# Kernel tuning notes

Measured on AMD Instinct MI355X. Metric: run time of the kernel, lower is better.

Reference implementation:

```python
import jax, jax.numpy as jnp
import numpy as np
import math

B, S, E = 16, 600, 300   # batch, seq_len, enc_len
H, NC = 512, 2           # hidden, classes
D = S * E                # archi[0] = 180000


def setup_inputs() -> dict:
    key = jax.random.key(0)
    ks = jax.random.split(key, 7)
    x = jax.random.normal(ks[0], (B, S, E), dtype=jnp.float32)
    y = jax.random.randint(ks[1], (B,), 0, NC)
    # neurons initialized to zeros (init_neurons)
    n0 = jnp.zeros((B, S, E), jnp.float32)
    n1 = jnp.zeros((B, H), jnp.float32)
    n2 = jnp.zeros((B, NC), jnp.float32)
    # Linear weights (torch layout: [out, in]), Kaiming-uniform-like scale 1/sqrt(fan_in)
    W0 = jax.random.uniform(ks[2], (E, E), jnp.float32, -1.0, 1.0) / math.sqrt(E)
    W1 = jax.random.uniform(ks[3], (H, D), jnp.float32, -1.0, 1.0) / math.sqrt(D)
    b1 = jax.random.uniform(ks[4], (H,), jnp.float32, -1.0, 1.0) / math.sqrt(D)
    W2 = jax.random.uniform(ks[5], (NC, H), jnp.float32, -1.0, 1.0) / math.sqrt(H)
    b2 = jax.random.uniform(ks[6], (NC,), jnp.float32, -1.0, 1.0) / math.sqrt(H)
    return dict(x=x, y=y, n0=n0, n1=n1, n2=n2, W0=W0, W1=W1, b1=b1, W2=W2, b2=b2, T=3)


def reference(x, y, n0, n1, n2, W0, W1, b1, W2, b2, T):
    # EqProp free-phase relaxation (beta = 0.0, forward default).
    # Analytic dPhi/dneurons replaces torch.autograd.grad:
    scale = 1.0 / math.sqrt(E)
    Wx = jnp.einsum('bse,fe->bsf', x, W0)  # synapses[0](x), constant across steps
    for _ in range(T):
        g0 = Wx + (n1 @ W1).reshape(B, S, E)              # dPhi/dn0
        g1 = n0.reshape(B, D) @ W1.T + b1 + n2 @ W2       # dPhi/dn1
        g2 = n1 @ W2.T + b2                               # dPhi/dn2 (beta=0)
        # hand-coded attention update for neuron 0: Q=g0, K=V=x
        attn = jax.nn.softmax(scale * jnp.einsum('bse,bte->bst', g0, x), axis=-1)
        n0 = jnp.einsum('bst,bte->bse', attn, x)
        n1 = jnp.tanh(g1)
        n2 = jnp.tanh(g2)
    return n0, n1, n2
```

## Files before the change

kernel.cpp:

```cpp
#include <hip/hip_runtime.h>
#include <math.h>

#define DD 180000L
#define HH 512
#define BB 16
#define SS 600
#define EE 300
#define SP 608
#define EP 320

typedef unsigned short u16;
typedef __attribute__((ext_vector_type(8))) __bf16 bf16x8;
typedef __attribute__((ext_vector_type(4))) float f32x4;

__device__ __forceinline__ u16 f2bf(float f) {
  union { float f; unsigned int u; } x; x.f = f;
  unsigned int r = (x.u + 0x7FFFu + ((x.u >> 16) & 1u)) >> 16;
  return (u16)r;
}

__global__ __launch_bounds__(256) void k_conv_x(const float* __restrict__ x,
                                                u16* __restrict__ xb, u16* __restrict__ xt) {
  __shared__ u16 tl[32][33];
  int b = blockIdx.z;
  int tt = blockIdx.x * 32, ee = blockIdx.y * 32;
  int lx = threadIdx.x & 31, ly = threadIdx.x >> 5;
#pragma unroll
  for (int i = 0; i < 4; ++i) {
    int t = tt + ly + i * 8, e = ee + lx;
    float v = (t < SS && e < EE) ? x[((long)b * SS + t) * EE + e] : 0.f;
    u16 h = f2bf(v);
    xb[((long)b * SP + t) * EP + e] = h;
    tl[ly + i * 8][lx] = h;
  }
  __syncthreads();
#pragma unroll
  for (int i = 0; i < 4; ++i) {
    int e = ee + ly + i * 8, t = tt + lx;
    xt[((long)b * EP + e) * SP + t] = tl[lx][ly + i * 8];
  }
}

__global__ __launch_bounds__(256) void k_conv_w0(const float* __restrict__ W0, u16* __restrict__ w0b) {
  int idx = blockIdx.x * 256 + threadIdx.x;
  int f = idx / EP, e = idx % EP;
  float v = (f < EE && e < EE) ? W0[f * EE + e] : 0.f;
  w0b[idx] = f2bf(v);
}

__global__ __launch_bounds__(256) void k_gemm_nt(
    const u16* __restrict__ A, int lda, long sA, int Arows,
    const u16* __restrict__ B, int ldb, long sB, int Brows,
    float* __restrict__ C, int ldc, long sC, int Mv, int Nv, int K,
    u16* __restrict__ Cb, int ldcb, long sCb) {
  int bz = blockIdx.z;
  int m0 = blockIdx.x * 64, n0 = blockIdx.y * 64;
  int lane = threadIdx.x & 63, wv = threadIdx.x >> 6;
  int wm = m0 + (wv >> 1) * 32, wn = n0 + (wv & 1) * 32;
  int q = lane >> 4, ln = lane & 15;
  const u16* Ab = A + (long)bz * sA;
  const u16* Bb = B + (long)bz * sB;
  long arow0 = (long)min(wm + ln, Arows - 1) * lda;
  long arow1 = (long)min(wm + 16 + ln, Arows - 1) * lda;
  long brow0 = (long)min(wn + ln, Brows - 1) * ldb;
  long brow1 = (long)min(wn + 16 + ln, Brows - 1) * ldb;
  f32x4 acc00 = {0.f,0.f,0.f,0.f}, acc01 = acc00, acc10 = acc00, acc11 = acc00;
  int ksteps = (K + 31) >> 5;
  for (int kk = 0; kk < ksteps; ++kk) {
    int k0 = kk * 32 + q * 8;
    bf16x8 a0 = *(const bf16x8*)(Ab + arow0 + k0);
    bf16x8 a1 = *(const bf16x8*)(Ab + arow1 + k0);
    bf16x8 b0 = *(const bf16x8*)(Bb + brow0 + k0);
    bf16x8 bv1 = *(const bf16x8*)(Bb + brow1 + k0);
    acc00 = __builtin_amdgcn_mfma_f32_16x16x32_bf16(a0, b0,  acc00, 0, 0, 0);
    acc01 = __builtin_amdgcn_mfma_f32_16x16x32_bf16(a0, bv1, acc01, 0, 0, 0);
    acc10 = __builtin_amdgcn_mfma_f32_16x16x32_bf16(a1, b0,  acc10, 0, 0, 0);
    acc11 = __builtin_amdgcn_mfma_f32_16x16x32_bf16(a1, bv1, acc11, 0, 0, 0);
  }
  float* Cp = C + (long)bz * sC;
  u16* Cbp = Cb ? (Cb + (long)bz * sCb) : (u16*)0;
#pragma unroll
  for (int sm = 0; sm < 2; ++sm) {
#pragma unroll
    for (int sn = 0; sn < 2; ++sn) {
      f32x4 acc = (sm == 0) ? ((sn == 0) ? acc00 : acc01) : ((sn == 0) ? acc10 : acc11);
#pragma unroll
      for (int r = 0; r < 4; ++r) {
        int m = wm + sm * 16 + q * 4 + r;
        int n = wn + sn * 16 + ln;
        if (m < Mv) {
          float v = acc[r];
          if (n < Nv) Cp[(long)m * ldc + n] = v;
          if (Cbp && n < ldcb) Cbp[(long)m * ldcb + n] = f2bf(n < Nv ? v : 0.f);
        }
      }
    }
  }
}

#define BN 256
#define BK 64
#define NCH 704

__global__ __launch_bounds__(256) void k_fused_w1(
    const float* __restrict__ W1, const float* __restrict__ n1f,
    const float* __restrict__ n0f, const float* __restrict__ Wx,
    u16* __restrict__ g0b, float* __restrict__ part) {
  __shared__ u16 wt[BK][BN + 8];
  __shared__ u16 n1s[BB][HH + 8];
  __shared__ u16 n0s[BB][BN + 8];
  int tid = threadIdx.x;
  long d0 = (long)blockIdx.x * BN;
#pragma unroll
  for (int i = 0; i < 8; ++i) {
    int f = i * 256 + tid;
    int b = f >> 7, c = (f & 127) * 4;
    float4 v = *(const float4*)(n1f + b * HH + c);
    n1s[b][c] = f2bf(v.x); n1s[b][c + 1] = f2bf(v.y);
    n1s[b][c + 2] = f2bf(v.z); n1s[b][c + 3] = f2bf(v.w);
  }
#pragma unroll
  for (int i = 0; i < 4; ++i) {
    int f = i * 256 + tid;
    int b = f >> 6, c = (f & 63) * 4;
    long d = d0 + c;
    float4 v = {0.f,0.f,0.f,0.f};
    if (d < DD) v = *(const float4*)(n0f + (long)b * DD + d);
    n0s[b][c] = f2bf(v.x); n0s[b][c + 1] = f2bf(v.y);
    n0s[b][c + 2] = f2bf(v.z); n0s[b][c + 3] = f2bf(v.w);
  }
  int lane = tid & 63, wv = tid >> 6, q = lane >> 4, ln = lane & 15;
  f32x4 acc0[4] = {{0.f,0.f,0.f,0.f},{0.f,0.f,0.f,0.f},{0.f,0.f,0.f,0.f},{0.f,0.f,0.f,0.f}};

  float4 pre[16];
#pragma unroll
  for (int i = 0; i < 16; ++i) {
    int f = i * 256 + tid;
    int r = f >> 6, c = (f & 63) * 4;
    long d = d0 + c;
    float4 v = {0.f,0.f,0.f,0.f};
    if (d < DD) v = *(const float4*)(W1 + (long)r * DD + d);
    pre[i] = v;
  }
  for (int s = 0; s < 8; ++s) {
    int h0 = s * BK;
    __syncthreads();
#pragma unroll
    for (int i = 0; i < 16; ++i) {
      int f = i * 256 + tid;
      int r = f >> 6, c = (f & 63) * 4;
      wt[r][c] = f2bf(pre[i].x); wt[r][c + 1] = f2bf(pre[i].y);
      wt[r][c + 2] = f2bf(pre[i].z); wt[r][c + 3] = f2bf(pre[i].w);
    }
    if (s < 7) {
#pragma unroll
      for (int i = 0; i < 16; ++i) {
        int f = i * 256 + tid;
        int r = f >> 6, c = (f & 63) * 4;
        long d = d0 + c;
        float4 v = {0.f,0.f,0.f,0.f};
        if (d < DD) v = *(const float4*)(W1 + (long)(h0 + BK + r) * DD + d);
        pre[i] = v;
      }
    }
    __syncthreads();
#pragma unroll
    for (int kst = 0; kst < 2; ++kst) {
      bf16x8 af = *(const bf16x8*)(&n1s[ln][h0 + kst * 32 + q * 8]);
#pragma unroll
      for (int nt = 0; nt < 4; ++nt) {
        int dc = wv * 64 + nt * 16 + ln;
        bf16x8 bv;
#pragma unroll
        for (int j = 0; j < 8; ++j) bv[j] = *(const __bf16*)(&wt[kst * 32 + q * 8 + j][dc]);
        acc0[nt] = __builtin_amdgcn_mfma_f32_16x16x32_bf16(af, bv, acc0[nt], 0, 0, 0);
      }
    }
    f32x4 acc1 = {0.f,0.f,0.f,0.f};
#pragma unroll
    for (int kst = 0; kst < 8; ++kst) {
      bf16x8 af = *(const bf16x8*)(&n0s[ln][kst * 32 + q * 8]);
      bf16x8 bv = *(const bf16x8*)(&wt[wv * 16 + ln][kst * 32 + q * 8]);
      acc1 = __builtin_amdgcn_mfma_f32_16x16x32_bf16(af, bv, acc1, 0, 0, 0);
    }
    long pb = (long)blockIdx.x * 8192;
#pragma unroll
    for (int r = 0; r < 4; ++r) {
      int b = q * 4 + r, h = h0 + wv * 16 + ln;
      part[pb + b * HH + h] = acc1[r];
    }
  }
#pragma unroll
  for (int nt = 0; nt < 4; ++nt) {
#pragma unroll
    for (int r = 0; r < 4; ++r) {
      int b = q * 4 + r;
      long d = d0 + wv * 64 + nt * 16 + ln;
      if (d < DD) {
        float val = Wx[(long)b * DD + d] + acc0[nt][r];
        int sI = (int)(d / EE), e = (int)(d % EE);
        g0b[((long)b * SS + sI) * EP + e] = f2bf(val);
      }
    }
  }
}

__global__ __launch_bounds__(256) void k_flash(const u16* __restrict__ g0b,
                                               const u16* __restrict__ xb,
                                               const u16* __restrict__ xt,
                                               float* __restrict__ out_n0, float scale) {
  __shared__ u16 Qs[16][328];
  __shared__ float Ss[16][609];
  __shared__ u16 Ps[16][616];
  int qt = blockIdx.x, b = blockIdx.y;
  int tid = threadIdx.x, lane = tid & 63, wv = tid >> 6, q = lane >> 4, ln = lane & 15;

#pragma unroll
  for (int i = 0; i < 3; ++i) {
    int c = tid + i * 256;
    if (c < 640) {
      int row = c / 40, cg = (c % 40) * 8;
      int qrow = min(qt * 16 + row, SS - 1);
      bf16x8 v = *(const bf16x8*)(g0b + ((long)b * SS + qrow) * EP + cg);
#pragma unroll
      for (int j = 0; j < 8; ++j) if (cg + j >= EE) v[j] = (__bf16)0.f;
      *(bf16x8*)&Qs[row][cg] = v;
    }
  }
  __syncthreads();

  f32x4 sacc[10];
#pragma unroll
  for (int i = 0; i < 10; ++i) sacc[i] = (f32x4){0.f,0.f,0.f,0.f};
  for (int k = 0; k < 10; ++k) {
    bf16x8 af = *(const bf16x8*)&Qs[ln][k * 32 + q * 8];
#pragma unroll
    for (int nt = 0; nt < 10; ++nt) {
      int tile = nt * 4 + wv;
      if (tile < 38) {
        bf16x8 bv = *(const bf16x8*)(xb + ((long)b * SP + tile * 16 + ln) * EP + k * 32 + q * 8);
        sacc[nt] = __builtin_amdgcn_mfma_f32_16x16x32_bf16(af, bv, sacc[nt], 0, 0, 0);
      }
    }
  }
#pragma unroll
  for (int nt = 0; nt < 10; ++nt) {
    int tile = nt * 4 + wv;
    if (tile < 38) {
#pragma unroll
      for (int r = 0; r < 4; ++r)
        Ss[q * 4 + r][tile * 16 + ln] = sacc[nt][r] * scale;
    }
  }
  __syncthreads();

#pragma unroll
  for (int r = 0; r < 4; ++r) {
    int row = wv * 4 + r;
    float v[10], mx = -1e30f;
#pragma unroll
    for (int i = 0; i < 10; ++i) {
      int c = lane + i * 64;
      v[i] = (c < SS) ? Ss[row][c] : -1e30f;
      mx = fmaxf(mx, v[i]);
    }
#pragma unroll
    for (int off = 1; off < 64; off <<= 1) mx = fmaxf(mx, __shfl_xor(mx, off));
    float sum = 0.f;
#pragma unroll
    for (int i = 0; i < 10; ++i) {
      int c = lane + i * 64;
      v[i] = (c < SS) ? __expf(v[i] - mx) : 0.f;
      sum += v[i];
    }
#pragma unroll
    for (int off = 1; off < 64; off <<= 1) sum += __shfl_xor(sum, off);
    float inv = 1.f / sum;
#pragma unroll
    for (int i = 0; i < 10; ++i) {
      int c = lane + i * 64;
      if (c < SP) Ps[row][c] = f2bf(v[i] * inv);
    }
  }
  __syncthreads();

  f32x4 oacc[5];
#pragma unroll
  for (int j = 0; j < 5; ++j) oacc[j] = (f32x4){0.f,0.f,0.f,0.f};
  for (int k = 0; k < 19; ++k) {
    bf16x8 af = *(const bf16x8*)&Ps[ln][k * 32 + q * 8];
#pragma unroll
    for (int j = 0; j < 5; ++j) {
      int e = (j * 4 + wv) * 16 + ln;
      bf16x8 bv = *(const bf16x8*)(xt + ((long)b * EP + e) * SP + k * 32 + q * 8);
      oacc[j] = __builtin_amdgcn_mfma_f32_16x16x32_bf16(af, bv, oacc[j], 0, 0, 0);
    }
  }
#pragma unroll
  for (int j = 0; j < 5; ++j) {
    int e = (j * 4 + wv) * 16 + ln;
    if (e < EE) {
#pragma unroll
      for (int r = 0; r < 4; ++r) {
        int qrow = qt * 16 + q * 4 + r;
        if (qrow < SS) out_n0[((long)b * SS + qrow) * EE + e] = oacc[j][r];
      }
    }
  }
}

__global__ __launch_bounds__(256) void k_init(const float* __restrict__ b1, const float* __restrict__ b2,
                                              float* __restrict__ n1, float* __restrict__ n2) {
  int idx = blockIdx.x * 256 + threadIdx.x;
  n1[idx] = tanhf(b1[idx & 511]);
  if (idx < 32) n2[idx] = tanhf(b2[idx & 1]);
}

__global__ __launch_bounds__(64) void k_g2(const float* __restrict__ n1old, const float* __restrict__ W2,
                                           const float* __restrict__ b2, float* __restrict__ n2out) {
  int b = blockIdx.x >> 1, c = blockIdx.x & 1, lane = threadIdx.x;
  float s = 0.f;
#pragma unroll
  for (int i = 0; i < 8; ++i) { int h = lane + i * 64; s += n1old[b * HH + h] * W2[c * HH + h]; }
  for (int off = 32; off; off >>= 1) s += __shfl_down(s, off);
  if (lane == 0) n2out[b * 2 + c] = tanhf(s + b2[c]);
}

__global__ __launch_bounds__(256) void k_reduce1(const float* __restrict__ part, float* __restrict__ part2) {
  int idx = blockIdx.x * 256 + threadIdx.x;
  int sl = blockIdx.y;
  float s = 0.f;
  int c0 = sl * 88;
#pragma unroll 4
  for (int c = 0; c < 88; ++c) s += part[(long)(c0 + c) * 8192 + idx];
  part2[(long)sl * 8192 + idx] = s;
}

__global__ __launch_bounds__(256) void k_reduce2(const float* __restrict__ part2, const float* __restrict__ b1,
                                                 const float* __restrict__ W2, const float* __restrict__ n2old,
                                                 float* __restrict__ n1out) {
  int idx = blockIdx.x * 256 + threadIdx.x;
  int b = idx >> 9, h = idx & 511;
  float s = b1[h] + n2old[b * 2] * W2[h] + n2old[b * 2 + 1] * W2[HH + h];
#pragma unroll
  for (int sl = 0; sl < 8; ++sl) s += part2[(long)sl * 8192 + idx];
  n1out[idx] = tanhf(s);
}

extern "C" void kernel_launch(void* const* d_in, const int* in_sizes, int n_in,
                              void* d_out, int out_size, void* d_ws, size_t ws_size,
                              hipStream_t stream) {
  const float* x  = (const float*)d_in[0];
  const float* W0 = (const float*)d_in[5];
  const float* W1 = (const float*)d_in[6];
  const float* b1 = (const float*)d_in[7];
  const float* W2 = (const float*)d_in[8];
  const float* b2 = (const float*)d_in[9];

  float* out_n0 = (float*)d_out;
  float* out_n1 = out_n0 + 16L * SS * EE;
  float* out_n2 = out_n1 + 16L * HH;

  char* w = (char*)d_ws;
  auto take = [&](size_t bytes) { char* p = w; w += (bytes + 255) & ~(size_t)255; return p; };
  u16*   xb    = (u16*)take(16L * SP * EP * 2);
  u16*   xt    = (u16*)take(16L * EP * SP * 2);
  u16*   w0b   = (u16*)take((size_t)EP * EP * 2);
  float* Wx    = (float*)take(16L * SS * EE * 4);
  u16*   g0b   = (u16*)take(16L * SS * EP * 2);
  float* part  = (float*)take((size_t)NCH * 8192 * 4);
  float* part2 = (float*)take(8L * 8192 * 4);
  float* n1A   = (float*)take(8192 * 4);
  float* n1B   = (float*)take(8192 * 4);
  float* n2A   = (float*)take(256);
  float* n2B   = (float*)take(256);

  const float scale = 1.0f / sqrtf((float)EE);

  k_conv_x<<<dim3(19, 10, 16), 256, 0, stream>>>(x, xb, xt);
  k_conv_w0<<<400, 256, 0, stream>>>(W0, w0b);
  k_gemm_nt<<<dim3(10, 5, 16), 256, 0, stream>>>(xb, EP, (long)SP * EP, SP,
                                                 w0b, EP, 0, EP,
                                                 Wx, EE, (long)SS * EE, SS, EE, EE,
                                                 g0b, EP, (long)SS * EP);
  k_init<<<32, 256, 0, stream>>>(b1, b2, n1A, n2A);

  for (int it = 0; it < 3; ++it) {
    if (it > 0) {
      const float* n1old = (it == 1) ? n1A : n1B;
      const float* n2old = (it == 1) ? n2A : n2B;
      float* n2new = (it == 1) ? n2B : out_n2;
      float* n1new = (it == 1) ? n1B : out_n1;
      k_g2<<<32, 64, 0, stream>>>(n1old, W2, b2, n2new);
      k_fused_w1<<<NCH, 256, 0, stream>>>(W1, n1old, out_n0, Wx, g0b, part);
      k_reduce1<<<dim3(32, 8), 256, 0, stream>>>(part, part2);
      k_reduce2<<<32, 256, 0, stream>>>(part2, b1, W2, n2old, n1new);
    }
    k_flash<<<dim3(38, 16), 256, 0, stream>>>(g0b, xb, xt, out_n0, scale);
  }
}
```

Measured before the change: 974.9 us.

## Replace partial-sum buffers with atomics and compute n1@W1 in fp32 FMA

The fused W1 kernel now accumulates the n0·W1ᵀ partial sums directly into a global n1pre buffer with atomicAdd. This removes the large per-block partial array and the two reduction kernels. The n1@W1 product is computed with fp32 vector FMAs from a transposed n1 copy staged in shared memory, replacing the bf16 MFMA path with its strided gather. The old register prefetch of W1 is replaced by direct per-half loads. The g2 kernel and the reductions are merged into a single tail kernel, which also writes the transposed n1 and re-zeros n1pre. In exchange, n1pre now depends on atomic contention and nondeterministic summation order, and the loads have less latency hiding.

```diff
diff --git a/kernel.cpp b/kernel.cpp
--- a/kernel.cpp
+++ b/kernel.cpp
@@ -10,6 +10,7 @@
 #define EP 320
 
 typedef unsigned short u16;
+typedef unsigned int u32;
 typedef __attribute__((ext_vector_type(8))) __bf16 bf16x8;
 typedef __attribute__((ext_vector_type(4))) float f32x4;
 
@@ -102,104 +103,114 @@
 #define BK 64
 #define NCH 704
 
+#define WT_PITCH 272
+#define N0_PITCH 264
+#define SM_WT    0
+#define SM_N0    34816
+#define SM_N1    43264
+#define SM_TOT   76032
+
 __global__ __launch_bounds__(256) void k_fused_w1(
-    const float* __restrict__ W1, const float* __restrict__ n1f,
+    const float* __restrict__ W1, const float* __restrict__ n1T,
     const float* __restrict__ n0f, const float* __restrict__ Wx,
-    u16* __restrict__ g0b, float* __restrict__ part) {
-  __shared__ u16 wt[BK][BN + 8];
-  __shared__ u16 n1s[BB][HH + 8];
-  __shared__ u16 n0s[BB][BN + 8];
-  int tid = threadIdx.x;
+    u16* __restrict__ g0b, float* __restrict__ n1pre) {
+  __shared__ char smem[SM_TOT];
+  u16*   wt  = (u16*)(smem + SM_WT);
+  u16*   n0s = (u16*)(smem + SM_N0);
+  float* n1s = (float*)(smem + SM_N1);
+  float* red = (float*)(smem + SM_WT);
+
+  int tid = threadIdx.x, w = tid >> 6, l = tid & 63;
+  int lane = tid & 63, q = lane >> 4, ln = lane & 15;
   long d0 = (long)blockIdx.x * BN;
-#pragma unroll
-  for (int i = 0; i < 8; ++i) {
-    int f = i * 256 + tid;
-    int b = f >> 7, c = (f & 127) * 4;
-    float4 v = *(const float4*)(n1f + b * HH + c);
-    n1s[b][c] = f2bf(v.x); n1s[b][c + 1] = f2bf(v.y);
-    n1s[b][c + 2] = f2bf(v.z); n1s[b][c + 3] = f2bf(v.w);
-  }
+  long colbase = d0 + 4 * l;
+
+#pragma unroll
+  for (int i = 0; i < 8; ++i)
+    ((f32x4*)n1s)[i * 256 + tid] = ((const f32x4*)n1T)[i * 256 + tid];
 #pragma unroll
   for (int i = 0; i < 4; ++i) {
     int f = i * 256 + tid;
     int b = f >> 6, c = (f & 63) * 4;
     long d = d0 + c;
-    float4 v = {0.f,0.f,0.f,0.f};
-    if (d < DD) v = *(const float4*)(n0f + (long)b * DD + d);
-    n0s[b][c] = f2bf(v.x); n0s[b][c + 1] = f2bf(v.y);
-    n0s[b][c + 2] = f2bf(v.z); n0s[b][c + 3] = f2bf(v.w);
-  }
-  int lane = tid & 63, wv = tid >> 6, q = lane >> 4, ln = lane & 15;
-  f32x4 acc0[4] = {{0.f,0.f,0.f,0.f},{0.f,0.f,0.f,0.f},{0.f,0.f,0.f,0.f},{0.f,0.f,0.f,0.f}};
-
-  float4 pre[16];
-#pragma unroll
-  for (int i = 0; i < 16; ++i) {
-    int f = i * 256 + tid;
-    int r = f >> 6, c = (f & 63) * 4;
-    long d = d0 + c;
-    float4 v = {0.f,0.f,0.f,0.f};
-    if (d < DD) v = *(const float4*)(W1 + (long)r * DD + d);
-    pre[i] = v;
-  }
+    f32x4 v = {0.f,0.f,0.f,0.f};
+    if (d < DD) v = *(const f32x4*)(n0f + (long)b * DD + d);
+    u32 lo = f2bf(v[0]) | ((u32)f2bf(v[1]) << 16);
+    u32 hi = f2bf(v[2]) | ((u32)f2bf(v[3]) << 16);
+    *(u32*)&n0s[b * N0_PITCH + c]     = lo;
+    *(u32*)&n0s[b * N0_PITCH + c + 2] = hi;
+  }
+
+  f32x4 acc0v[16];
+#pragma unroll
+  for (int b = 0; b < 16; ++b) acc0v[b] = (f32x4){0.f,0.f,0.f,0.f};
+
   for (int s = 0; s < 8; ++s) {
     int h0 = s * BK;
     __syncthreads();
 #pragma unroll
-    for (int i = 0; i < 16; ++i) {
-      int f = i * 256 + tid;
-      int r = f >> 6, c = (f & 63) * 4;
-      wt[r][c] = f2bf(pre[i].x); wt[r][c + 1] = f2bf(pre[i].y);
-      wt[r][c + 2] = f2bf(pre[i].z); wt[r][c + 3] = f2bf(pre[i].w);
-    }
-    if (s < 7) {
-#pragma unroll
-      for (int i = 0; i < 16; ++i) {
-        int f = i * 256 + tid;
-        int r = f >> 6, c = (f & 63) * 4;
-        long d = d0 + c;
-        float4 v = {0.f,0.f,0.f,0.f};
-        if (d < DD) v = *(const float4*)(W1 + (long)(h0 + BK + r) * DD + d);
-        pre[i] = v;
+    for (int half = 0; half < 2; ++half) {
+      f32x4 v[8];
+#pragma unroll
+      for (int i = 0; i < 8; ++i) {
+        int r = half * 32 + i * 4 + w;
+        v[i] = (colbase < DD) ? *(const f32x4*)(W1 + (long)(h0 + r) * DD + colbase)
+                              : (f32x4){0.f,0.f,0.f,0.f};
+      }
+#pragma unroll
+      for (int i = 0; i < 8; ++i) {
+        int r = half * 32 + i * 4 + w;
+        const float* nr = &n1s[(h0 + r) * 16];
+        f32x4 a0 = *(const f32x4*)(nr + 0);
+        f32x4 a1 = *(const f32x4*)(nr + 4);
+        f32x4 a2 = *(const f32x4*)(nr + 8);
+        f32x4 a3 = *(const f32x4*)(nr + 12);
+        acc0v[0]  += a0[0] * v[i];  acc0v[1]  += a0[1] * v[i];
+        acc0v[2]  += a0[2] * v[i];  acc0v[3]  += a0[3] * v[i];
+        acc0v[4]  += a1[0] * v[i];  acc0v[5]  += a1[1] * v[i];
+        acc0v[6]  += a1[2] * v[i];  acc0v[7]  += a1[3] * v[i];
+        acc0v[8]  += a2[0] * v[i];  acc0v[9]  += a2[1] * v[i];
+        acc0v[10] += a2[2] * v[i];  acc0v[11] += a2[3] * v[i];
+        acc0v[12] += a3[0] * v[i];  acc0v[13] += a3[1] * v[i];
+        acc0v[14] += a3[2] * v[i];  acc0v[15] += a3[3] * v[i];
+        u32 lo = f2bf(v[i][0]) | ((u32)f2bf(v[i][1]) << 16);
+        u32 hi = f2bf(v[i][2]) | ((u32)f2bf(v[i][3]) << 16);
+        *(u32*)&wt[r * WT_PITCH + 4 * l]     = lo;
+        *(u32*)&wt[r * WT_PITCH + 4 * l + 2] = hi;
       }
     }
     __syncthreads();
-#pragma unroll
-    for (int kst = 0; kst < 2; ++kst) {
-      bf16x8 af = *(const bf16x8*)(&n1s[ln][h0 + kst * 32 + q * 8]);
-#pragma unroll
-      for (int nt = 0; nt < 4; ++nt) {
-        int dc = wv * 64 + nt * 16 + ln;
-        bf16x8 bv;
-#pragma unroll
-        for (int j = 0; j < 8; ++j) bv[j] = *(const __bf16*)(&wt[kst * 32 + q * 8 + j][dc]);
-        acc0[nt] = __builtin_amdgcn_mfma_f32_16x16x32_bf16(af, bv, acc0[nt], 0, 0, 0);
-      }
-    }
     f32x4 acc1 = {0.f,0.f,0.f,0.f};
 #pragma unroll
     for (int kst = 0; kst < 8; ++kst) {
-      bf16x8 af = *(const bf16x8*)(&n0s[ln][kst * 32 + q * 8]);
-      bf16x8 bv = *(const bf16x8*)(&wt[wv * 16 + ln][kst * 32 + q * 8]);
+      bf16x8 af = *(const bf16x8*)&n0s[ln * N0_PITCH + kst * 32 + q * 8];
+      bf16x8 bv = *(const bf16x8*)&wt[(w * 16 + ln) * WT_PITCH + kst * 32 + q * 8];
       acc1 = __builtin_amdgcn_mfma_f32_16x16x32_bf16(af, bv, acc1, 0, 0, 0);
     }
-    long pb = (long)blockIdx.x * 8192;
 #pragma unroll
     for (int r = 0; r < 4; ++r) {
-      int b = q * 4 + r, h = h0 + wv * 16 + ln;
-      part[pb + b * HH + h] = acc1[r];
-    }
-  }
-#pragma unroll
-  for (int nt = 0; nt < 4; ++nt) {
-#pragma unroll
-    for (int r = 0; r < 4; ++r) {
-      int b = q * 4 + r;
-      long d = d0 + wv * 64 + nt * 16 + ln;
-      if (d < DD) {
-        float val = Wx[(long)b * DD + d] + acc0[nt][r];
+      int b = q * 4 + r, h = h0 + w * 16 + ln;
+      atomicAdd(&n1pre[b * HH + h], acc1[r]);
+    }
+  }
+  for (int p = 0; p < 4; ++p) {
+    __syncthreads();
+#pragma unroll
+    for (int j = 0; j < 4; ++j)
+      *(f32x4*)&red[(w * 64 + l) * 20 + j * 4] = acc0v[p * 4 + j];
+    __syncthreads();
+    f32x4 sum = *(const f32x4*)&red[(0 * 64 + l) * 20 + w * 4];
+    sum += *(const f32x4*)&red[(1 * 64 + l) * 20 + w * 4];
+    sum += *(const f32x4*)&red[(2 * 64 + l) * 20 + w * 4];
+    sum += *(const f32x4*)&red[(3 * 64 + l) * 20 + w * 4];
+    int b = p * 4 + w;
+    if (colbase < DD) {
+      f32x4 wx = *(const f32x4*)(Wx + (long)b * DD + colbase);
+#pragma unroll
+      for (int j = 0; j < 4; ++j) {
+        long d = colbase + j;
         int sI = (int)(d / EE), e = (int)(d % EE);
-        g0b[((long)b * SS + sI) * EP + e] = f2bf(val);
+        g0b[((long)b * SS + sI) * EP + e] = f2bf(wx[j] + sum[j]);
       }
     }
   }
@@ -310,41 +321,36 @@
 }
 
 __global__ __launch_bounds__(256) void k_init(const float* __restrict__ b1, const float* __restrict__ b2,
-                                              float* __restrict__ n1, float* __restrict__ n2) {
-  int idx = blockIdx.x * 256 + threadIdx.x;
-  n1[idx] = tanhf(b1[idx & 511]);
-  if (idx < 32) n2[idx] = tanhf(b2[idx & 1]);
-}
-
-__global__ __launch_bounds__(64) void k_g2(const float* __restrict__ n1old, const float* __restrict__ W2,
-                                           const float* __restrict__ b2, float* __restrict__ n2out) {
-  int b = blockIdx.x >> 1, c = blockIdx.x & 1, lane = threadIdx.x;
-  float s = 0.f;
-#pragma unroll
-  for (int i = 0; i < 8; ++i) { int h = lane + i * 64; s += n1old[b * HH + h] * W2[c * HH + h]; }
-  for (int off = 32; off; off >>= 1) s += __shfl_down(s, off);
-  if (lane == 0) n2out[b * 2 + c] = tanhf(s + b2[c]);
-}
-
-__global__ __launch_bounds__(256) void k_reduce1(const float* __restrict__ part, float* __restrict__ part2) {
-  int idx = blockIdx.x * 256 + threadIdx.x;
-  int sl = blockIdx.y;
-  float s = 0.f;
-  int c0 = sl * 88;
-#pragma unroll 4
-  for (int c = 0; c < 88; ++c) s += part[(long)(c0 + c) * 8192 + idx];
-  part2[(long)sl * 8192 + idx] = s;
-}
-
-__global__ __launch_bounds__(256) void k_reduce2(const float* __restrict__ part2, const float* __restrict__ b1,
-                                                 const float* __restrict__ W2, const float* __restrict__ n2old,
-                                                 float* __restrict__ n1out) {
+                                              float* __restrict__ n1, float* __restrict__ n1T,
+                                              float* __restrict__ n2, float* __restrict__ n1pre) {
   int idx = blockIdx.x * 256 + threadIdx.x;
   int b = idx >> 9, h = idx & 511;
-  float s = b1[h] + n2old[b * 2] * W2[h] + n2old[b * 2 + 1] * W2[HH + h];
-#pragma unroll
-  for (int sl = 0; sl < 8; ++sl) s += part2[(long)sl * 8192 + idx];
-  n1out[idx] = tanhf(s);
+  float v = tanhf(b1[h]);
+  n1[idx] = v;
+  n1T[h * 16 + b] = v;
+  n1pre[idx] = 0.f;
+  if (idx < 32) n2[idx] = tanhf(b2[idx & 1]);
+}
+
+__global__ __launch_bounds__(256) void k_tail(const float* __restrict__ n1pre, const float* __restrict__ b1,
+                                              const float* __restrict__ W2, const float* __restrict__ b2,
+                                              const float* __restrict__ n1old, const float* __restrict__ n2old,
+                                              float* __restrict__ n1new, float* __restrict__ n2new,
+                                              float* __restrict__ n1T, float* __restrict__ n1pre_z) {
+  if (blockIdx.x < 32) {
+    int idx = blockIdx.x * 256 + threadIdx.x;
+    int b = idx >> 9, h = idx & 511;
+    float s = n1pre[idx] + b1[h] + n2old[b * 2] * W2[h] + n2old[b * 2 + 1] * W2[HH + h];
+    float v = tanhf(s);
+    n1new[idx] = v;
+    n1T[h * 16 + b] = v;
+    n1pre_z[idx] = 0.f;
+  } else if (threadIdx.x < 32) {
+    int b = threadIdx.x >> 1, c = threadIdx.x & 1;
+    float s = 0.f;
+    for (int h = 0; h < HH; ++h) s += n1old[b * HH + h] * W2[c * HH + h];
+    n2new[b * 2 + c] = tanhf(s + b2[c]);
+  }
 }
 
 extern "C" void kernel_launch(void* const* d_in, const int* in_sizes, int n_in,
@@ -368,8 +374,8 @@
   u16*   w0b   = (u16*)take((size_t)EP * EP * 2);
   float* Wx    = (float*)take(16L * SS * EE * 4);
   u16*   g0b   = (u16*)take(16L * SS * EP * 2);
-  float* part  = (float*)take((size_t)NCH * 8192 * 4);
-  float* part2 = (float*)take(8L * 8192 * 4);
+  float* n1pre = (float*)take(8192 * 4);
+  float* n1T   = (float*)take(8192 * 4);
   float* n1A   = (float*)take(8192 * 4);
   float* n1B   = (float*)take(8192 * 4);
   float* n2A   = (float*)take(256);
@@ -383,18 +389,17 @@
                                                  w0b, EP, 0, EP,
                                                  Wx, EE, (long)SS * EE, SS, EE, EE,
                                                  g0b, EP, (long)SS * EP);
-  k_init<<<32, 256, 0, stream>>>(b1, b2, n1A, n2A);
+  k_init<<<32, 256, 0, stream>>>(b1, b2, n1A, n1T, n2A, n1pre);
 
   for (int it = 0; it < 3; ++it) {
     if (it > 0) {
       const float* n1old = (it == 1) ? n1A : n1B;
       const float* n2old = (it == 1) ? n2A : n2B;
+      float* n1new = (it == 1) ? n1B : out_n1;
       float* n2new = (it == 1) ? n2B : out_n2;
-      float* n1new = (it == 1) ? n1B : out_n1;
-      k_g2<<<32, 64, 0, stream>>>(n1old, W2, b2, n2new);
-      k_fused_w1<<<NCH, 256, 0, stream>>>(W1, n1old, out_n0, Wx, g0b, part);
-      k_reduce1<<<dim3(32, 8), 256, 0, stream>>>(part, part2);
-      k_reduce2<<<32, 256, 0, stream>>>(part2, b1, W2, n2old, n1new);
+      k_fused_w1<<<NCH, 256, 0, stream>>>(W1, n1T, out_n0, Wx, g0b, n1pre);
+      k_tail<<<33, 256, 0, stream>>>(n1pre, b1, W2, b2, n1old, n2old,
+                                     n1new, n2new, n1T, n1pre);
     }
     k_flash<<<dim3(38, 16), 256, 0, stream>>>(g0b, xb, xt, out_n0, scale);
   }
```

New measurement: 1.034 ms. +6.0%, slower.
